# Kernel tuning notes

Hardware: AMD Instinct MI355X
Metric: run time of the kernel (lower is better)

The kernel has to match this reference:

```python
import jax, jax.numpy as jnp
from jax import lax
import numpy as np

IN_F, H1, OUT_F, P = 128, 64, 64, 0.25
B, T = 64, 2048


def setup_inputs() -> dict:
    key = jax.random.key(0)
    ks = jax.random.split(key, 12)
    def w(k, shape, fan_in):
        return jax.random.normal(k, shape, dtype=jnp.float32) / np.sqrt(fan_in).astype(np.float32)
    x = jax.random.normal(ks[0], (B, T, IN_F), dtype=jnp.float32)
    # PyTorch LSTM param layout: W_ih [4H, in], W_hh [4H, H], gate order i,f,g,o
    W_ih1 = w(ks[1], (4 * H1, IN_F), IN_F)
    W_hh1 = w(ks[2], (4 * H1, H1), H1)
    b_ih1 = jnp.zeros((4 * H1,), jnp.float32)
    b_hh1 = jnp.zeros((4 * H1,), jnp.float32)
    W_ih2 = w(ks[3], (4 * OUT_F, H1), H1)
    W_hh2 = w(ks[4], (4 * OUT_F, OUT_F), OUT_F)
    b_ih2 = jnp.zeros((4 * OUT_F,), jnp.float32)
    b_hh2 = jnp.zeros((4 * OUT_F,), jnp.float32)
    # Variational (locked) dropout masks: one per sequence, shared across timesteps,
    # inverted-dropout pre-scaled by 1/(1-p).
    keep = 1.0 - P
    mask1 = (jax.random.bernoulli(ks[5], keep, (B, H1)).astype(jnp.float32) / keep)
    mask2 = (jax.random.bernoulli(ks[6], keep, (B, OUT_F)).astype(jnp.float32) / keep)
    return {"x": x, "W_ih1": W_ih1, "W_hh1": W_hh1, "b_ih1": b_ih1, "b_hh1": b_hh1,
            "W_ih2": W_ih2, "W_hh2": W_hh2, "b_ih2": b_ih2, "b_hh2": b_hh2,
            "mask1": mask1, "mask2": mask2}


def _lstm(x, W_ih, W_hh, b_ih, b_hh):
    # x: [B,T,I]; returns all hidden states [B,T,H]
    Bd = x.shape[0]
    H = W_hh.shape[1]
    # Precompute input contribution for all timesteps (one big GEMM).
    xg = jnp.einsum('bti,gi->btg', x, W_ih) + b_ih + b_hh  # [B,T,4H]
    W_hh_T = W_hh.T  # [H,4H]
    def step(carry, xg_t):
        h, c = carry
        g = xg_t + h @ W_hh_T
        i, f, gg, o = jnp.split(g, 4, axis=-1)
        c = jax.nn.sigmoid(f) * c + jax.nn.sigmoid(i) * jnp.tanh(gg)
        h = jax.nn.sigmoid(o) * jnp.tanh(c)
        return (h, c), h
    h0 = jnp.zeros((Bd, H), x.dtype)
    c0 = jnp.zeros((Bd, H), x.dtype)
    _, hs = lax.scan(step, (h0, c0), jnp.swapaxes(xg, 0, 1))
    return jnp.swapaxes(hs, 0, 1)


def reference(x, W_ih1, W_hh1, b_ih1, b_hh1, W_ih2, W_hh2, b_ih2, b_hh2, mask1, mask2):
    out = _lstm(x, W_ih1, W_hh1, b_ih1, b_hh1) * mask1[:, None, :]
    out = _lstm(out, W_ih2, W_hh2, b_ih2, b_hh2) * mask2[:, None, :]
    return jax.nn.relu(out)
```

## Files before the change

### kernel.cpp

```cpp
#include <hip/hip_runtime.h>
#include <hip/hip_bf16.h>

#define BB 64
#define TT 2048
#define INF 128
#define HH 64
#define GG 256

__device__ __forceinline__ float sigm(float x) { return 1.0f / (1.0f + __expf(-x)); }
__device__ __forceinline__ float tanh_f(float x) {
  float e = __expf(2.0f * x);
  return 1.0f - 2.0f / (e + 1.0f);
}

#define WLD1(A_, P_, I_)                                                     \
  { float4 q = (P_)[I_];                                                     \
    A_[4*(I_)] = q.x; A_[4*(I_)+1] = q.y; A_[4*(I_)+2] = q.z; A_[4*(I_)+3] = q.w; }
#define WLD16(A_, P_) WLD1(A_,P_,0) WLD1(A_,P_,1) WLD1(A_,P_,2) WLD1(A_,P_,3) \
  WLD1(A_,P_,4) WLD1(A_,P_,5) WLD1(A_,P_,6) WLD1(A_,P_,7) WLD1(A_,P_,8)      \
  WLD1(A_,P_,9) WLD1(A_,P_,10) WLD1(A_,P_,11) WLD1(A_,P_,12) WLD1(A_,P_,13)  \
  WLD1(A_,P_,14) WLD1(A_,P_,15)

#define HRD1(I_) hb[I_] = Hb[I_];
#define HRD16 HRD1(0) HRD1(1) HRD1(2) HRD1(3) HRD1(4) HRD1(5) HRD1(6) HRD1(7) \
  HRD1(8) HRD1(9) HRD1(10) HRD1(11) HRD1(12) HRD1(13) HRD1(14) HRD1(15)

#define DG1(J_)                                                              \
  { float4 h4 = hb[J_];                                                      \
    aA0 = fmaf(h4.x, wa[4*(J_)],   aA0); aB0 = fmaf(h4.x, wb[4*(J_)],   aB0);\
    aA1 = fmaf(h4.y, wa[4*(J_)+1], aA1); aB1 = fmaf(h4.y, wb[4*(J_)+1], aB1);\
    aA0 = fmaf(h4.z, wa[4*(J_)+2], aA0); aB0 = fmaf(h4.z, wb[4*(J_)+2], aB0);\
    aA1 = fmaf(h4.w, wa[4*(J_)+3], aA1); aB1 = fmaf(h4.w, wb[4*(J_)+3], aB1); }
#define DG16 DG1(0) DG1(1) DG1(2) DG1(3) DG1(4) DG1(5) DG1(6) DG1(7)          \
  DG1(8) DG1(9) DG1(10) DG1(11) DG1(12) DG1(13) DG1(14) DG1(15)

#define XW1(I)                                                     \
  { float4 a = Wp[(I)];                                            \
    w[4*(I)] = a.x; w[4*(I)+1] = a.y; w[4*(I)+2] = a.z; w[4*(I)+3] = a.w; }
#define XW4(I) XW1(I) XW1((I)+1) XW1((I)+2) XW1((I)+3)
#define XWLOAD XW4(0) XW4(4) XW4(8) XW4(12) XW4(16) XW4(20) XW4(24) XW4(28)

#define GR1(B_, BASE_, I_) B_[I_] = Xb4[(BASE_) + (I_)];
#define GR8(B_, BASE_) GR1(B_,BASE_,0) GR1(B_,BASE_,1) GR1(B_,BASE_,2)       \
  GR1(B_,BASE_,3) GR1(B_,BASE_,4) GR1(B_,BASE_,5) GR1(B_,BASE_,6) GR1(B_,BASE_,7)
#define GF1(B_, WB_, I_)                                                     \
  { float4 h4 = B_[I_];                                                      \
    a0 = fmaf(h4.x, w[(WB_)+4*(I_)],   a0); a1 = fmaf(h4.y, w[(WB_)+4*(I_)+1], a1); \
    a2 = fmaf(h4.z, w[(WB_)+4*(I_)+2], a2); a3 = fmaf(h4.w, w[(WB_)+4*(I_)+3], a3); }
#define GF8(B_, WB_) GF1(B_,WB_,0) GF1(B_,WB_,1) GF1(B_,WB_,2) GF1(B_,WB_,3) \
  GF1(B_,WB_,4) GF1(B_,WB_,5) GF1(B_,WB_,6) GF1(B_,WB_,7)

__global__ __launch_bounds__(256, 1) void xgemm(const float* __restrict__ X,
                                                const float* __restrict__ W,
                                                const float* __restrict__ bi,
                                                const float* __restrict__ bh,
                                                float* __restrict__ XG) {
  __shared__ __align__(16) float Xs[64 * INF];
  const int t = threadIdx.x;
  const long m0 = (long)blockIdx.x * 256;

  float w[INF];
  const float4* Wp = (const float4*)(W + (size_t)t * INF);
  XWLOAD
  const float bias = bi[t] + bh[t];

  for (int tile = 0; tile < 4; ++tile) {
    const float4* src = (const float4*)(X + (size_t)(m0 + tile * 64) * INF);
#pragma unroll
    for (int i = 0; i < 8; ++i) {
      int idx = t + i * 256;
      ((float4*)Xs)[idx] = src[idx];
    }
    __syncthreads();
    for (int r = 0; r < 64; ++r) {
      const float4* Xb4 = (const float4*)&Xs[r * INF];
      float4 ba[8], bb[8];
      float a0 = bias, a1 = 0.f, a2 = 0.f, a3 = 0.f;
      GR8(ba, 0) GR8(bb, 8)
      GF8(ba, 0)
      GR8(ba, 16)
      GF8(bb, 32)
      GR8(bb, 24)
      GF8(ba, 64)
      GF8(bb, 96)
      XG[(size_t)(m0 + tile * 64 + r) * GG + t] = (a0 + a1) + (a2 + a3);
    }
    __syncthreads();
  }
}

__global__ __launch_bounds__(384, 1) void lstm2(const float* __restrict__ XG,
                                                const float* __restrict__ Whh1,
                                                const float* __restrict__ Wih2,
                                                const float* __restrict__ Whh2,
                                                const float* __restrict__ bi2,
                                                const float* __restrict__ bh2,
                                                const float* __restrict__ m1g,
                                                const float* __restrict__ m2g,
                                                float* __restrict__ out) {
  const int b = blockIdx.x;
  const int wid = threadIdx.x >> 6;
  const int lane = threadIdx.x & 63;

  __shared__ int fh1, fb, fc1, fc2, fh2, fe;
  __shared__ __align__(16) float h1loc[HH];
  __shared__ __align__(16) float h2loc[HH];
  __shared__ __align__(16) float x2buf[4][HH];
  __shared__ __align__(16) float gob1[4][2 * HH];
  __shared__ __align__(16) float gob2[4][2 * HH];
  __shared__ __align__(16) float a2x[4][GG];

  if (threadIdx.x == 0) { fh1 = 0; fb = 0; fc1 = 0; fc2 = 0; fh2 = 0; fe = 0; }
  if (threadIdx.x < HH) h1loc[threadIdx.x] = 0.f;
  else if (threadIdx.x < 2 * HH) h2loc[threadIdx.x - HH] = 0.f;
  __syncthreads();

#define WAIT_GE(flag, tgt)                                   \
  do {                                                       \
    while (*(volatile int*)&(flag) < (tgt)) {}               \
    asm volatile("" ::: "memory");                           \
  } while (0)
#define PUBLISH(flag, val)                                   \
  do {                                                       \
    asm volatile("s_waitcnt lgkmcnt(0)" ::: "memory");       \
    if (lane == 0) *(volatile int*)&(flag) = (val);          \
  } while (0)

  if (wid == 2) {
    const float4* pa = (const float4*)(Whh1 + (size_t)lane * HH);
    const float4* pb = (const float4*)(Whh1 + (size_t)(64 + lane) * HH);
    float wa[HH], wb[HH];
    WLD16(wa, pa) WLD16(wb, pb)
    const float m1 = m1g[b * HH + lane];
    const float* xgp = XG + (size_t)b * TT * GG;

    float c1 = 0.f;
    float cur_i = xgp[lane], cur_f = xgp[64 + lane];
    float n1_i = xgp[GG + lane], n1_f = xgp[GG + 64 + lane];
    for (int s = 0; s < TT; ++s) {
      float n2_i = 0.f, n2_f = 0.f;
      if (s + 2 < TT) {
        const float* q = xgp + (size_t)(s + 2) * GG;
        n2_i = q[lane]; n2_f = q[64 + lane];
      }
      const float4* Hb = (const float4*)h1loc;
      float4 hb[16];
      HRD16
      float aA0 = cur_i, aA1 = 0.f, aB0 = cur_f, aB1 = 0.f;
      DG16
      WAIT_GE(fb, s + 1);
      float ag = gob1[s & 3][lane];
      float ao = gob1[s & 3][64 + lane];
      WAIT_GE(fc1, s - 3); WAIT_GE(fc2, s - 3);
      float ai = aA0 + aA1, af = aB0 + aB1;
      c1 = sigm(af) * c1 + sigm(ai) * tanh_f(ag);
      float h1 = sigm(ao) * tanh_f(c1);
      h1loc[lane] = h1;
      x2buf[s & 3][lane] = h1 * m1;
      PUBLISH(fh1, s + 1);
      cur_i = n1_i; cur_f = n1_f; n1_i = n2_i; n1_f = n2_f;
    }
  } else if (wid == 0) {
    const float4* pa = (const float4*)(Whh1 + (size_t)(128 + lane) * HH);
    const float4* pb = (const float4*)(Whh1 + (size_t)(192 + lane) * HH);
    float wa[HH], wb[HH];
    WLD16(wa, pa) WLD16(wb, pb)
    const float* xgp = XG + (size_t)b * TT * GG;

    float cur_g = xgp[128 + lane], cur_o = xgp[192 + lane];
    float n1_g = xgp[GG + 128 + lane], n1_o = xgp[GG + 192 + lane];
    for (int s = 0; s < TT; ++s) {
      float n2_g = 0.f, n2_o = 0.f;
      if (s + 2 < TT) {
        const float* q = xgp + (size_t)(s + 2) * GG;
        n2_g = q[128 + lane]; n2_o = q[192 + lane];
      }
      WAIT_GE(fh1, s);
      const float4* Hb = (const float4*)h1loc;
      float4 hb[16];
      HRD16
      float aA0 = cur_g, aA1 = 0.f, aB0 = cur_o, aB1 = 0.f;
      DG16
      gob1[s & 3][lane] = aA0 + aA1;
      gob1[s & 3][64 + lane] = aB0 + aB1;
      PUBLISH(fb, s + 1);
      cur_g = n1_g; cur_o = n1_o; n1_g = n2_g; n1_o = n2_o;
    }
  } else if (wid == 1 || wid == 5) {
    const int r0 = (wid == 1) ? 0 : 128;
    const float4* pa = (const float4*)(Wih2 + (size_t)(r0 + lane) * HH);
    const float4* pb = (const float4*)(Wih2 + (size_t)(r0 + 64 + lane) * HH);
    float wa[HH], wb[HH];
    WLD16(wa, pa) WLD16(wb, pb)
    const float bias_a = bi2[r0 + lane] + bh2[r0 + lane];
    const float bias_b = bi2[r0 + 64 + lane] + bh2[r0 + 64 + lane];

    for (int s = 0; s < TT; ++s) {
      WAIT_GE(fh1, s + 1);
      const float4* Hb = (const float4*)x2buf[s & 3];
      float4 hb[16];
      HRD16
      float aA0 = bias_a, aA1 = 0.f, aB0 = bias_b, aB1 = 0.f;
      DG16
      WAIT_GE(fh2, s - 3);
      a2x[s & 3][r0 + lane] = aA0 + aA1;
      a2x[s & 3][r0 + 64 + lane] = aB0 + aB1;
      if (wid == 1) { PUBLISH(fc1, s + 1); } else { PUBLISH(fc2, s + 1); }
    }
  } else if (wid == 4) {
    const float4* pa = (const float4*)(Whh2 + (size_t)(128 + lane) * HH);
    const float4* pb = (const float4*)(Whh2 + (size_t)(192 + lane) * HH);
    float wa[HH], wb[HH];
    WLD16(wa, pa) WLD16(wb, pb)

    for (int s = 0; s < TT; ++s) {
      WAIT_GE(fh2, s);
      const float4* Hb = (const float4*)h2loc;
      float4 hb[16];
      HRD16
      float aA0 = 0.f, aA1 = 0.f, aB0 = 0.f, aB1 = 0.f;
      DG16
      gob2[s & 3][lane] = aA0 + aA1;
      gob2[s & 3][64 + lane] = aB0 + aB1;
      PUBLISH(fe, s + 1);
    }
  } else {
    const float4* pa = (const float4*)(Whh2 + (size_t)lane * HH);
    const float4* pb = (const float4*)(Whh2 + (size_t)(64 + lane) * HH);
    float wa[HH], wb[HH];
    WLD16(wa, pa) WLD16(wb, pb)
    const float m2 = m2g[b * HH + lane];
    float* ob = out + (size_t)b * TT * HH;

    float c2 = 0.f;
    for (int s = 0; s < TT; ++s) {
      const float4* Hb = (const float4*)h2loc;
      float4 hb[16];
      HRD16
      float aA0 = 0.f, aA1 = 0.f, aB0 = 0.f, aB1 = 0.f;
      DG16
      WAIT_GE(fe, s + 1);
      WAIT_GE(fc1, s + 1); WAIT_GE(fc2, s + 1);
      float ai = aA0 + aA1 + a2x[s & 3][lane];
      float af = aB0 + aB1 + a2x[s & 3][64 + lane];
      float ag = gob2[s & 3][lane] + a2x[s & 3][128 + lane];
      float ao = gob2[s & 3][64 + lane] + a2x[s & 3][192 + lane];
      c2 = sigm(af) * c2 + sigm(ai) * tanh_f(ag);
      float h2 = sigm(ao) * tanh_f(c2);
      h2loc[lane] = h2;
      PUBLISH(fh2, s + 1);
      ob[(size_t)s * HH + lane] = fmaxf(h2 * m2, 0.f);
    }
  }
#undef WAIT_GE
#undef PUBLISH
}

extern "C" void kernel_launch(void* const* d_in, const int* in_sizes, int n_in,
                              void* d_out, int out_size, void* d_ws, size_t ws_size,
                              hipStream_t stream) {
  (void)in_sizes; (void)n_in; (void)out_size; (void)ws_size;
  const float* x     = (const float*)d_in[0];
  const float* W_ih1 = (const float*)d_in[1];
  const float* W_hh1 = (const float*)d_in[2];
  const float* b_ih1 = (const float*)d_in[3];
  const float* b_hh1 = (const float*)d_in[4];
  const float* W_ih2 = (const float*)d_in[5];
  const float* W_hh2 = (const float*)d_in[6];
  const float* b_ih2 = (const float*)d_in[7];
  const float* b_hh2 = (const float*)d_in[8];
  const float* mask1 = (const float*)d_in[9];
  const float* mask2 = (const float*)d_in[10];
  float* out = (float*)d_out;

  float* xg1 = (float*)d_ws;

  xgemm<<<dim3(BB * TT / 256), dim3(256), 0, stream>>>(x, W_ih1, b_ih1, b_hh1, xg1);
  lstm2<<<dim3(BB), dim3(384), 0, stream>>>(xg1, W_hh1, W_ih2, W_hh2, b_ih2, b_hh2,
                                            mask1, mask2, out);
}
```

Before: 2.758 ms.

## Broadcast hidden state via readlane and replicate cell update across gate waves

```diff
diff --git a/kernel.cpp b/kernel.cpp
--- a/kernel.cpp
+++ b/kernel.cpp
@@ -12,6 +12,7 @@
   float e = __expf(2.0f * x);
   return 1.0f - 2.0f / (e + 1.0f);
 }
+#define RL(v, l) __uint_as_float(__builtin_amdgcn_readlane(__float_as_uint(v), (l)))
 
 #define WLD1(A_, P_, I_)                                                     \
   { float4 q = (P_)[I_];                                                     \
@@ -21,18 +22,12 @@
   WLD1(A_,P_,9) WLD1(A_,P_,10) WLD1(A_,P_,11) WLD1(A_,P_,12) WLD1(A_,P_,13)  \
   WLD1(A_,P_,14) WLD1(A_,P_,15)
 
-#define HRD1(I_) hb[I_] = Hb[I_];
-#define HRD16 HRD1(0) HRD1(1) HRD1(2) HRD1(3) HRD1(4) HRD1(5) HRD1(6) HRD1(7) \
-  HRD1(8) HRD1(9) HRD1(10) HRD1(11) HRD1(12) HRD1(13) HRD1(14) HRD1(15)
-
-#define DG1(J_)                                                              \
-  { float4 h4 = hb[J_];                                                      \
-    aA0 = fmaf(h4.x, wa[4*(J_)],   aA0); aB0 = fmaf(h4.x, wb[4*(J_)],   aB0);\
-    aA1 = fmaf(h4.y, wa[4*(J_)+1], aA1); aB1 = fmaf(h4.y, wb[4*(J_)+1], aB1);\
-    aA0 = fmaf(h4.z, wa[4*(J_)+2], aA0); aB0 = fmaf(h4.z, wb[4*(J_)+2], aB0);\
-    aA1 = fmaf(h4.w, wa[4*(J_)+3], aA1); aB1 = fmaf(h4.w, wb[4*(J_)+3], aB1); }
-#define DG16 DG1(0) DG1(1) DG1(2) DG1(3) DG1(4) DG1(5) DG1(6) DG1(7)          \
-  DG1(8) DG1(9) DG1(10) DG1(11) DG1(12) DG1(13) DG1(14) DG1(15)
+#define LD2(K)                                                               \
+  { float h0_ = RL(hreg, (K)); float h1_ = RL(hreg, (K)+1);                  \
+    aA0 = fmaf(h0_, wa[(K)],   aA0); aB0 = fmaf(h0_, wb[(K)],   aB0);        \
+    aA1 = fmaf(h1_, wa[(K)+1], aA1); aB1 = fmaf(h1_, wb[(K)+1], aB1); }
+#define LD8(K) LD2(K) LD2((K)+2) LD2((K)+4) LD2((K)+6)
+#define DOT64 LD8(0) LD8(8) LD8(16) LD8(24) LD8(32) LD8(40) LD8(48) LD8(56)
 
 #define XW1(I)                                                     \
   { float4 a = Wp[(I)];                                            \
@@ -40,23 +35,21 @@
 #define XW4(I) XW1(I) XW1((I)+1) XW1((I)+2) XW1((I)+3)
 #define XWLOAD XW4(0) XW4(4) XW4(8) XW4(12) XW4(16) XW4(20) XW4(24) XW4(28)
 
-#define GR1(B_, BASE_, I_) B_[I_] = Xb4[(BASE_) + (I_)];
-#define GR8(B_, BASE_) GR1(B_,BASE_,0) GR1(B_,BASE_,1) GR1(B_,BASE_,2)       \
-  GR1(B_,BASE_,3) GR1(B_,BASE_,4) GR1(B_,BASE_,5) GR1(B_,BASE_,6) GR1(B_,BASE_,7)
-#define GF1(B_, WB_, I_)                                                     \
-  { float4 h4 = B_[I_];                                                      \
-    a0 = fmaf(h4.x, w[(WB_)+4*(I_)],   a0); a1 = fmaf(h4.y, w[(WB_)+4*(I_)+1], a1); \
-    a2 = fmaf(h4.z, w[(WB_)+4*(I_)+2], a2); a3 = fmaf(h4.w, w[(WB_)+4*(I_)+3], a3); }
-#define GF8(B_, WB_) GF1(B_,WB_,0) GF1(B_,WB_,1) GF1(B_,WB_,2) GF1(B_,WB_,3) \
-  GF1(B_,WB_,4) GF1(B_,WB_,5) GF1(B_,WB_,6) GF1(B_,WB_,7)
-
-__global__ __launch_bounds__(256, 1) void xgemm(const float* __restrict__ X,
+#define XD2(L)                                                     \
+  { float xa_ = RL(cx, (L)); float xb_ = RL(cy, (L));              \
+    a0 = fmaf(xa_, w[2*(L)],   a0); a1 = fmaf(xb_, w[2*(L)+1], a1);\
+    float xc_ = RL(cx, (L)+1); float xd_ = RL(cy, (L)+1);          \
+    a2 = fmaf(xc_, w[2*(L)+2], a2); a3 = fmaf(xd_, w[2*(L)+3], a3); }
+#define XD8(L) XD2(L) XD2((L)+2) XD2((L)+4) XD2((L)+6)
+#define XDOT64 XD8(0) XD8(8) XD8(16) XD8(24) XD8(32) XD8(40) XD8(48) XD8(56)
+
+__global__ __launch_bounds__(256, 2) void xgemm(const float* __restrict__ X,
                                                 const float* __restrict__ W,
                                                 const float* __restrict__ bi,
                                                 const float* __restrict__ bh,
                                                 float* __restrict__ XG) {
-  __shared__ __align__(16) float Xs[64 * INF];
   const int t = threadIdx.x;
+  const int lane = t & 63;
   const long m0 = (long)blockIdx.x * 256;
 
   float w[INF];
@@ -64,28 +57,19 @@
   XWLOAD
   const float bias = bi[t] + bh[t];
 
-  for (int tile = 0; tile < 4; ++tile) {
-    const float4* src = (const float4*)(X + (size_t)(m0 + tile * 64) * INF);
-#pragma unroll
-    for (int i = 0; i < 8; ++i) {
-      int idx = t + i * 256;
-      ((float4*)Xs)[idx] = src[idx];
-    }
-    __syncthreads();
-    for (int r = 0; r < 64; ++r) {
-      const float4* Xb4 = (const float4*)&Xs[r * INF];
-      float4 ba[8], bb[8];
-      float a0 = bias, a1 = 0.f, a2 = 0.f, a3 = 0.f;
-      GR8(ba, 0) GR8(bb, 8)
-      GF8(ba, 0)
-      GR8(ba, 16)
-      GF8(bb, 32)
-      GR8(bb, 24)
-      GF8(ba, 64)
-      GF8(bb, 96)
-      XG[(size_t)(m0 + tile * 64 + r) * GG + t] = (a0 + a1) + (a2 + a3);
-    }
-    __syncthreads();
+  const float2* Xp = (const float2*)X;
+  float2 cur = Xp[(size_t)m0 * 64 + lane];
+  float2 nx1 = Xp[(size_t)(m0 + 1) * 64 + lane];
+
+  for (int mi = 0; mi < 256; ++mi) {
+    const long m = m0 + mi;
+    float2 nx2 = (mi + 2 < 256) ? Xp[(size_t)(m + 2) * 64 + lane] : cur;
+
+    const float cx = cur.x, cy = cur.y;
+    float a0 = bias, a1 = 0.f, a2 = 0.f, a3 = 0.f;
+    XDOT64
+    XG[(size_t)m * GG + t] = (a0 + a1) + (a2 + a3);
+    cur = nx1; nx1 = nx2;
   }
 }
 
@@ -102,17 +86,18 @@
   const int wid = threadIdx.x >> 6;
   const int lane = threadIdx.x & 63;
 
-  __shared__ int fh1, fb, fc1, fc2, fh2, fe;
-  __shared__ __align__(16) float h1loc[HH];
-  __shared__ __align__(16) float h2loc[HH];
+  __shared__ int fAd, fBd, fh1, fc, fc2, fDd, fEd, fDu, fEu;
+  __shared__ __align__(16) float d1if[2][2 * HH];
+  __shared__ __align__(16) float d1go[2][2 * HH];
+  __shared__ __align__(16) float d2if[2][2 * HH];
+  __shared__ __align__(16) float d2go[2][2 * HH];
   __shared__ __align__(16) float x2buf[4][HH];
-  __shared__ __align__(16) float gob1[4][2 * HH];
-  __shared__ __align__(16) float gob2[4][2 * HH];
-  __shared__ __align__(16) float a2x[4][GG];
-
-  if (threadIdx.x == 0) { fh1 = 0; fb = 0; fc1 = 0; fc2 = 0; fh2 = 0; fe = 0; }
-  if (threadIdx.x < HH) h1loc[threadIdx.x] = 0.f;
-  else if (threadIdx.x < 2 * HH) h2loc[threadIdx.x - HH] = 0.f;
+  __shared__ __align__(16) float a2if[4][2 * HH];
+  __shared__ __align__(16) float a2go[4][2 * HH];
+
+  if (threadIdx.x == 0) {
+    fAd = 0; fBd = 0; fh1 = 0; fc = 0; fc2 = 0; fDd = 0; fEd = 0; fDu = 0; fEu = 0;
+  }
   __syncthreads();
 
 #define WAIT_GE(flag, tgt)                                   \
@@ -126,130 +111,152 @@
     if (lane == 0) *(volatile int*)&(flag) = (val);          \
   } while (0)
 
-  if (wid == 2) {
-    const float4* pa = (const float4*)(Whh1 + (size_t)lane * HH);
-    const float4* pb = (const float4*)(Whh1 + (size_t)(64 + lane) * HH);
-    float wa[HH], wb[HH];
-    WLD16(wa, pa) WLD16(wb, pb)
+  if (wid == 0) {
+    float wa[HH], wb[HH];
+    { const float4* P1 = (const float4*)(Whh1 + (size_t)lane * HH);
+      const float4* P2 = (const float4*)(Whh1 + (size_t)(64 + lane) * HH);
+      WLD16(wa, P1) WLD16(wb, P2) }
     const float m1 = m1g[b * HH + lane];
     const float* xgp = XG + (size_t)b * TT * GG;
 
-    float c1 = 0.f;
     float cur_i = xgp[lane], cur_f = xgp[64 + lane];
     float n1_i = xgp[GG + lane], n1_f = xgp[GG + 64 + lane];
+    float hreg = 0.f, c1 = 0.f;
     for (int s = 0; s < TT; ++s) {
       float n2_i = 0.f, n2_f = 0.f;
       if (s + 2 < TT) {
         const float* q = xgp + (size_t)(s + 2) * GG;
         n2_i = q[lane]; n2_f = q[64 + lane];
       }
-      const float4* Hb = (const float4*)h1loc;
-      float4 hb[16];
-      HRD16
       float aA0 = cur_i, aA1 = 0.f, aB0 = cur_f, aB1 = 0.f;
-      DG16
-      WAIT_GE(fb, s + 1);
-      float ag = gob1[s & 3][lane];
-      float ao = gob1[s & 3][64 + lane];
-      WAIT_GE(fc1, s - 3); WAIT_GE(fc2, s - 3);
+      DOT64
+      d1if[s & 1][lane] = aA0 + aA1;
+      d1if[s & 1][64 + lane] = aB0 + aB1;
+      PUBLISH(fAd, s + 1);
+      WAIT_GE(fBd, s + 1);
+      float ag = d1go[s & 1][lane], ao = d1go[s & 1][64 + lane];
       float ai = aA0 + aA1, af = aB0 + aB1;
       c1 = sigm(af) * c1 + sigm(ai) * tanh_f(ag);
-      float h1 = sigm(ao) * tanh_f(c1);
-      h1loc[lane] = h1;
-      x2buf[s & 3][lane] = h1 * m1;
+      hreg = sigm(ao) * tanh_f(c1);
+      WAIT_GE(fc, s - 2); WAIT_GE(fc2, s - 2);
+      x2buf[s & 3][lane] = hreg * m1;
       PUBLISH(fh1, s + 1);
       cur_i = n1_i; cur_f = n1_f; n1_i = n2_i; n1_f = n2_f;
     }
-  } else if (wid == 0) {
-    const float4* pa = (const float4*)(Whh1 + (size_t)(128 + lane) * HH);
-    const float4* pb = (const float4*)(Whh1 + (size_t)(192 + lane) * HH);
-    float wa[HH], wb[HH];
-    WLD16(wa, pa) WLD16(wb, pb)
+  } else if (wid == 1) {
+    float wa[HH], wb[HH];
+    { const float4* P1 = (const float4*)(Whh1 + (size_t)(128 + lane) * HH);
+      const float4* P2 = (const float4*)(Whh1 + (size_t)(192 + lane) * HH);
+      WLD16(wa, P1) WLD16(wb, P2) }
     const float* xgp = XG + (size_t)b * TT * GG;
 
     float cur_g = xgp[128 + lane], cur_o = xgp[192 + lane];
     float n1_g = xgp[GG + 128 + lane], n1_o = xgp[GG + 192 + lane];
+    float hreg = 0.f, c1 = 0.f;
     for (int s = 0; s < TT; ++s) {
       float n2_g = 0.f, n2_o = 0.f;
       if (s + 2 < TT) {
         const float* q = xgp + (size_t)(s + 2) * GG;
         n2_g = q[128 + lane]; n2_o = q[192 + lane];
       }
-      WAIT_GE(fh1, s);
-      const float4* Hb = (const float4*)h1loc;
-      float4 hb[16];
-      HRD16
       float aA0 = cur_g, aA1 = 0.f, aB0 = cur_o, aB1 = 0.f;
-      DG16
-      gob1[s & 3][lane] = aA0 + aA1;
-      gob1[s & 3][64 + lane] = aB0 + aB1;
-      PUBLISH(fb, s + 1);
+      DOT64
+      d1go[s & 1][lane] = aA0 + aA1;
+      d1go[s & 1][64 + lane] = aB0 + aB1;
+      PUBLISH(fBd, s + 1);
+      WAIT_GE(fAd, s + 1);
+      float ai = d1if[s & 1][lane], af = d1if[s & 1][64 + lane];
+      float ag = aA0 + aA1, ao = aB0 + aB1;
+      c1 = sigm(af) * c1 + sigm(ai) * tanh_f(ag);
+      hreg = sigm(ao) * tanh_f(c1);
       cur_g = n1_g; cur_o = n1_o; n1_g = n2_g; n1_o = n2_o;
     }
-  } else if (wid == 1 || wid == 5) {
-    const int r0 = (wid == 1) ? 0 : 128;
-    const float4* pa = (const float4*)(Wih2 + (size_t)(r0 + lane) * HH);
-    const float4* pb = (const float4*)(Wih2 + (size_t)(r0 + 64 + lane) * HH);
-    float wa[HH], wb[HH];
-    WLD16(wa, pa) WLD16(wb, pb)
-    const float bias_a = bi2[r0 + lane] + bh2[r0 + lane];
-    const float bias_b = bi2[r0 + 64 + lane] + bh2[r0 + 64 + lane];
-
-    for (int s = 0; s < TT; ++s) {
-      WAIT_GE(fh1, s + 1);
-      const float4* Hb = (const float4*)x2buf[s & 3];
-      float4 hb[16];
-      HRD16
-      float aA0 = bias_a, aA1 = 0.f, aB0 = bias_b, aB1 = 0.f;
-      DG16
-      WAIT_GE(fh2, s - 3);
-      a2x[s & 3][r0 + lane] = aA0 + aA1;
-      a2x[s & 3][r0 + 64 + lane] = aB0 + aB1;
-      if (wid == 1) { PUBLISH(fc1, s + 1); } else { PUBLISH(fc2, s + 1); }
-    }
-  } else if (wid == 4) {
-    const float4* pa = (const float4*)(Whh2 + (size_t)(128 + lane) * HH);
-    const float4* pb = (const float4*)(Whh2 + (size_t)(192 + lane) * HH);
-    float wa[HH], wb[HH];
-    WLD16(wa, pa) WLD16(wb, pb)
-
-    for (int s = 0; s < TT; ++s) {
-      WAIT_GE(fh2, s);
-      const float4* Hb = (const float4*)h2loc;
-      float4 hb[16];
-      HRD16
-      float aA0 = 0.f, aA1 = 0.f, aB0 = 0.f, aB1 = 0.f;
-      DG16
-      gob2[s & 3][lane] = aA0 + aA1;
-      gob2[s & 3][64 + lane] = aB0 + aB1;
-      PUBLISH(fe, s + 1);
-    }
-  } else {
-    const float4* pa = (const float4*)(Whh2 + (size_t)lane * HH);
-    const float4* pb = (const float4*)(Whh2 + (size_t)(64 + lane) * HH);
-    float wa[HH], wb[HH];
-    WLD16(wa, pa) WLD16(wb, pb)
+  } else if (wid == 2) {
+    float wa[HH], wb[HH];
+    { const float4* P1 = (const float4*)(Whh2 + (size_t)lane * HH);
+      const float4* P2 = (const float4*)(Whh2 + (size_t)(64 + lane) * HH);
+      WLD16(wa, P1) WLD16(wb, P2) }
     const float m2 = m2g[b * HH + lane];
     float* ob = out + (size_t)b * TT * HH;
 
-    float c2 = 0.f;
-    for (int s = 0; s < TT; ++s) {
-      const float4* Hb = (const float4*)h2loc;
-      float4 hb[16];
-      HRD16
+    float hreg = 0.f, c2 = 0.f;
+    for (int s = 0; s < TT; ++s) {
       float aA0 = 0.f, aA1 = 0.f, aB0 = 0.f, aB1 = 0.f;
-      DG16
-      WAIT_GE(fe, s + 1);
-      WAIT_GE(fc1, s + 1); WAIT_GE(fc2, s + 1);
-      float ai = aA0 + aA1 + a2x[s & 3][lane];
-      float af = aB0 + aB1 + a2x[s & 3][64 + lane];
-      float ag = gob2[s & 3][lane] + a2x[s & 3][128 + lane];
-      float ao = gob2[s & 3][64 + lane] + a2x[s & 3][192 + lane];
+      DOT64
+      d2if[s & 1][lane] = aA0 + aA1;
+      d2if[s & 1][64 + lane] = aB0 + aB1;
+      PUBLISH(fDd, s + 1);
+      WAIT_GE(fEd, s + 1);
+      float dg = d2go[s & 1][lane], do_ = d2go[s & 1][64 + lane];
+      WAIT_GE(fc, s + 1); WAIT_GE(fc2, s + 1);
+      float ai = aA0 + aA1 + a2if[s & 3][lane];
+      float af = aB0 + aB1 + a2if[s & 3][64 + lane];
+      float ag = dg + a2go[s & 3][lane];
+      float ao = do_ + a2go[s & 3][64 + lane];
       c2 = sigm(af) * c2 + sigm(ai) * tanh_f(ag);
-      float h2 = sigm(ao) * tanh_f(c2);
-      h2loc[lane] = h2;
-      PUBLISH(fh2, s + 1);
-      ob[(size_t)s * HH + lane] = fmaxf(h2 * m2, 0.f);
+      hreg = sigm(ao) * tanh_f(c2);
+      ob[(size_t)s * HH + lane] = fmaxf(hreg * m2, 0.f);
+      PUBLISH(fDu, s + 1);
+    }
+  } else if (wid == 3) {
+    float wa[HH], wb[HH];
+    { const float4* P1 = (const float4*)(Whh2 + (size_t)(128 + lane) * HH);
+      const float4* P2 = (const float4*)(Whh2 + (size_t)(192 + lane) * HH);
+      WLD16(wa, P1) WLD16(wb, P2) }
+
+    float hreg = 0.f, c2 = 0.f;
+    for (int s = 0; s < TT; ++s) {
+      float aA0 = 0.f, aA1 = 0.f, aB0 = 0.f, aB1 = 0.f;
+      DOT64
+      d2go[s & 1][lane] = aA0 + aA1;
+      d2go[s & 1][64 + lane] = aB0 + aB1;
+      PUBLISH(fEd, s + 1);
+      WAIT_GE(fDd, s + 1);
+      float di = d2if[s & 1][lane], df = d2if[s & 1][64 + lane];
+      WAIT_GE(fc, s + 1); WAIT_GE(fc2, s + 1);
+      float ai = di + a2if[s & 3][lane];
+      float af = df + a2if[s & 3][64 + lane];
+      float ag = aA0 + aA1 + a2go[s & 3][lane];
+      float ao = aB0 + aB1 + a2go[s & 3][64 + lane];
+      c2 = sigm(af) * c2 + sigm(ai) * tanh_f(ag);
+      hreg = sigm(ao) * tanh_f(c2);
+      PUBLISH(fEu, s + 1);
+    }
+  } else if (wid == 4) {
+    float wa[HH], wb[HH];
+    { const float4* P1 = (const float4*)(Wih2 + (size_t)lane * HH);
+      const float4* P2 = (const float4*)(Wih2 + (size_t)(64 + lane) * HH);
+      WLD16(wa, P1) WLD16(wb, P2) }
+    const float bia = bi2[lane] + bh2[lane];
+    const float bib = bi2[64 + lane] + bh2[64 + lane];
+
+    for (int s = 0; s < TT; ++s) {
+      WAIT_GE(fh1, s + 1);
+      float hreg = x2buf[s & 3][lane];
+      float aA0 = bia, aA1 = 0.f, aB0 = bib, aB1 = 0.f;
+      DOT64
+      WAIT_GE(fDu, s - 2); WAIT_GE(fEu, s - 2);
+      a2if[s & 3][lane] = aA0 + aA1;
+      a2if[s & 3][64 + lane] = aB0 + aB1;
+      PUBLISH(fc, s + 1);
+    }
+  } else {
+    float wa[HH], wb[HH];
+    { const float4* P1 = (const float4*)(Wih2 + (size_t)(128 + lane) * HH);
+      const float4* P2 = (const float4*)(Wih2 + (size_t)(192 + lane) * HH);
+      WLD16(wa, P1) WLD16(wb, P2) }
+    const float bia = bi2[128 + lane] + bh2[128 + lane];
+    const float bib = bi2[192 + lane] + bh2[192 + lane];
+
+    for (int s = 0; s < TT; ++s) {
+      WAIT_GE(fh1, s + 1);
+      float hreg = x2buf[s & 3][lane];
+      float aA0 = bia, aA1 = 0.f, aB0 = bib, aB1 = 0.f;
+      DOT64
+      WAIT_GE(fDu, s - 2); WAIT_GE(fEu, s - 2);
+      a2go[s & 3][lane] = aA0 + aA1;
+      a2go[s & 3][64 + lane] = aB0 + aB1;
+      PUBLISH(fc2, s + 1);
     }
   }
 #undef WAIT_GE
```

Result: faster. 2.579 ms (-6.5%).
